# Optimization experiments

Measured on AMD Instinct MI355X. Metric: run time of the kernel, lower is better.

The kernel has to match this reference:

```python
import jax, jax.numpy as jnp
import numpy as np

B, S, D, H = 2, 2048, 1024, 16
HD = D // H  # head_dim = 64


def setup_inputs() -> dict:
    key = jax.random.key(0)
    k1, k2, k3, k4, k5 = jax.random.split(key, 5)
    x = jax.random.normal(k1, (B, S, D), dtype=jnp.float32)
    # causal additive mask [S, S]: 0 on/below diagonal, -1e9 above
    mask = jnp.where(jnp.tril(jnp.ones((S, S), dtype=bool)), 0.0, -1e9).astype(jnp.float32)
    scale = 1.0 / np.sqrt(D)
    W_qkv = jax.random.normal(k2, (D, 3 * D), dtype=jnp.float32) * scale
    b_qkv = jax.random.normal(k3, (3 * D,), dtype=jnp.float32) * 0.01
    W_o = jax.random.normal(k4, (D, D), dtype=jnp.float32) * scale
    b_o = jax.random.normal(k5, (D,), dtype=jnp.float32) * 0.01
    return {"x": x, "mask": mask, "W_qkv": W_qkv, "b_qkv": b_qkv, "W_o": W_o, "b_o": b_o}


def reference(x, mask, W_qkv, b_qkv, W_o, b_o):
    b, s, d = x.shape
    qkv = x @ W_qkv + b_qkv                         # [B,S,3D]
    qkv = qkv.reshape(b, s, H, 3 * HD).transpose(0, 2, 1, 3)  # [B,H,S,3*HD]
    q, k, v = jnp.split(qkv, 3, axis=-1)            # each [B,H,S,HD]
    scores = jnp.einsum('bhqd,bhkd->bhqk', q, k) / np.sqrt(HD)  # [B,H,S,S]
    scores = scores + mask                           # broadcast [S,S] additive mask
    attn = jax.nn.softmax(scores, axis=-1)
    vals = jnp.einsum('bhqk,bhkd->bhqd', attn, v)    # [B,H,S,HD]
    vals = vals.transpose(0, 2, 1, 3).reshape(b, s, d)
    return vals @ W_o + b_o
```

## Files before the change

### kernel.cpp

```cpp
#include <hip/hip_runtime.h>

#define NB 2
#define NS 2048
#define ND 1024
#define NH 16
#define NHD 64
#define QLD (3 * ND)
#define PADP 72

typedef unsigned short u16;
typedef __attribute__((ext_vector_type(8))) short short8;
typedef __attribute__((ext_vector_type(4))) float f32x4;

__device__ __forceinline__ u16 f2b(float f) {
    unsigned int x = __float_as_uint(f);
    return (u16)((x + 0x7fffu + ((x >> 16) & 1u)) >> 16);
}

__device__ __forceinline__ unsigned int cvtpk(float lo, float hi) {
    unsigned int r;
    asm("v_cvt_pk_bf16_f32 %0, %1, %2" : "=v"(r) : "v"(lo), "v"(hi));
    return r;
}

__device__ __forceinline__ int swz8(int d) {
    return ((d >> 1) ^ (d >> 3)) & 7;
}

__global__ __launch_bounds__(256) void prep(
    const float* __restrict__ x, u16* __restrict__ x_bf,
    const float* __restrict__ Wqkv, u16* __restrict__ WqkvT,
    const float* __restrict__ Wo, u16* __restrict__ WoT)
{
    __shared__ u16 Ts[64 * 72];
    const int bid = blockIdx.x;
    const int t = threadIdx.x;

    if (bid < 2048) {
        const int i = (bid * 256 + t) * 8;
        float4 a = *(const float4*)(x + i);
        float4 b = *(const float4*)(x + i + 4);
        *(ushort4*)(x_bf + i)     = make_ushort4(f2b(a.x), f2b(a.y), f2b(a.z), f2b(a.w));
        *(ushort4*)(x_bf + i + 4) = make_ushort4(f2b(b.x), f2b(b.y), f2b(b.z), f2b(b.w));
        return;
    }

    const float* W; u16* WT; int N, bx, by;
    if (bid < 2048 + 768) {
        const int r = bid - 2048;
        W = Wqkv; WT = WqkvT; N = QLD; bx = r % 48; by = r / 48;
    } else {
        const int r = bid - 2816;
        W = Wo; WT = WoT; N = ND; bx = r & 15; by = r >> 4;
    }
    const int K = ND;
    const int k0 = by << 6, n0 = bx << 6;
    const int rr0 = t >> 4, c = (t & 15) << 2;
    #pragma unroll
    for (int rr = 0; rr < 64; rr += 16) {
        float4 v = *(const float4*)&W[(size_t)(k0 + rr0 + rr) * N + n0 + c];
        Ts[(c + 0) * 72 + rr0 + rr] = f2b(v.x);
        Ts[(c + 1) * 72 + rr0 + rr] = f2b(v.y);
        Ts[(c + 2) * 72 + rr0 + rr] = f2b(v.z);
        Ts[(c + 3) * 72 + rr0 + rr] = f2b(v.w);
    }
    __syncthreads();
    const int n = t >> 2, cc = (t & 3) << 4;
    uint4 a = *(const uint4*)&Ts[n * 72 + cc];
    uint4 b = *(const uint4*)&Ts[n * 72 + cc + 8];
    *(uint4*)&WT[(size_t)(n0 + n) * K + k0 + cc]     = a;
    *(uint4*)&WT[(size_t)(n0 + n) * K + k0 + cc + 8] = b;
}

template <int BM, int BN, bool STORE_BF16>
__global__ __launch_bounds__(256) void gemm_mfma(
    const u16* __restrict__ A, const u16* __restrict__ BT,
    const float* __restrict__ bias,
    void* __restrict__ C, int M, int N, int K)
{
    constexpr int AIS = BM / 64;
    constexpr int BIS = BN / 64;
    constexpr int MI  = BM / 32;
    constexpr int NJ  = BN / 32;
    __shared__ u16 As[BM * 32];
    __shared__ u16 Bs[BN * 32];

    const int tid = threadIdx.x;
    const int wave = tid >> 6, lane = tid & 63;
    const int col = lane & 15, quad = lane >> 4;
    const int wm = wave >> 1, wn = wave & 1;

    const int nwgx = gridDim.x;
    const int wg = blockIdx.y * nwgx + blockIdx.x;
    const int cpx = (nwgx * gridDim.y) >> 3;
    const int swz = (wg & 7) * cpx + (wg >> 3);
    const int row0 = (swz / nwgx) * BM, col0 = (swz % nwgx) * BN;

    f32x4 acc[MI][NJ] = {};

    const u16* asrc[AIS];
    u16* adst[AIS];
    #pragma unroll
    for (int is = 0; is < AIS; ++is) {
        const int J = is * 256 + wave * 64 + lane;
        const int m = J >> 2;
        const int q = (J & 3) ^ ((m >> 1) & 3);
        asrc[is] = A + (size_t)(row0 + m) * K + q * 8;
        adst[is] = &As[(size_t)(is * 256 + wave * 64) * 8];
    }
    const u16* bsrc[BIS];
    u16* bdst[BIS];
    #pragma unroll
    for (int is = 0; is < BIS; ++is) {
        const int J = is * 256 + wave * 64 + lane;
        const int m = J >> 2;
        const int q = (J & 3) ^ ((m >> 1) & 3);
        bsrc[is] = BT + (size_t)(col0 + m) * K + q * 8;
        bdst[is] = &Bs[(size_t)(is * 256 + wave * 64) * 8];
    }

    for (int kk = 0; kk < K; kk += 32) {
        __syncthreads();
        #pragma unroll
        for (int is = 0; is < AIS; ++is)
            __builtin_amdgcn_global_load_lds(
                (const __attribute__((address_space(1))) unsigned int*)(asrc[is] + kk),
                (__attribute__((address_space(3))) unsigned int*)adst[is], 16, 0, 0);
        #pragma unroll
        for (int is = 0; is < BIS; ++is)
            __builtin_amdgcn_global_load_lds(
                (const __attribute__((address_space(1))) unsigned int*)(bsrc[is] + kk),
                (__attribute__((address_space(3))) unsigned int*)bdst[is], 16, 0, 0);
        __syncthreads();

        short8 af[MI], bf[NJ];
        #pragma unroll
        for (int i = 0; i < MI; ++i) {
            const int m = wm * (BM / 2) + i * 16 + col;
            af[i] = *(const short8*)&As[(m * 4 + (quad ^ ((m >> 1) & 3))) * 8];
        }
        #pragma unroll
        for (int j = 0; j < NJ; ++j) {
            const int n = wn * (BN / 2) + j * 16 + col;
            bf[j] = *(const short8*)&Bs[(n * 4 + (quad ^ ((n >> 1) & 3))) * 8];
        }
        #pragma unroll
        for (int i = 0; i < MI; ++i)
            #pragma unroll
            for (int j = 0; j < NJ; ++j)
                acc[i][j] = __builtin_amdgcn_mfma_f32_16x16x32_bf16(
                    af[i], bf[j], acc[i][j], 0, 0, 0);
    }

    #pragma unroll
    for (int j = 0; j < NJ; ++j) {
        const int gc = col0 + wn * (BN / 2) + j * 16 + col;
        const float bj = bias[gc];
        #pragma unroll
        for (int i = 0; i < MI; ++i) {
            const int gr = row0 + wm * (BM / 2) + i * 16 + quad * 4;
            #pragma unroll
            for (int r = 0; r < 4; ++r) {
                const float v = acc[i][j][r] + bj;
                if (STORE_BF16)
                    ((u16*)C)[(size_t)(gr + r) * N + gc] = f2b(v);
                else
                    ((float*)C)[(size_t)(gr + r) * N + gc] = v;
            }
        }
    }
}

__global__ __launch_bounds__(256) void attn_kernel(
    const u16* __restrict__ qkv, u16* __restrict__ vals)
{
    __shared__ u16 Ks[2][64 * 64];
    __shared__ u16 Vt[2][64 * 64];
    __shared__ u16 Ps[64 * PADP];

    const int tid = threadIdx.x;
    const int wave = tid >> 6, lane = tid & 63;
    const int col = lane & 15, quad = lane >> 4;
    const int qtA = blockIdx.x;
    const int qtB = 31 - qtA;
    const int bh = blockIdx.y;
    const int b = bh >> 4, h = bh & 15;
    const size_t base = (size_t)b * NS * QLD + (size_t)h * (3 * NHD);
    const int qloc = wave * 16 + col;

    int Jrow[2], Jcol[2];
    #pragma unroll
    for (int is = 0; is < 2; ++is) {
        const int J = is * 256 + wave * 64 + lane;
        Jrow[is] = J >> 3;
        Jcol[is] = ((J & 7) ^ (Jrow[is] & 7)) << 3;
    }

    auto stage_tile = [&](int buf, int srow, int coloff) {
        #pragma unroll
        for (int is = 0; is < 2; ++is) {
            __builtin_amdgcn_global_load_lds(
                (const __attribute__((address_space(1))) unsigned int*)
                    (qkv + base + (size_t)(srow + Jrow[is]) * QLD + coloff + Jcol[is]),
                (__attribute__((address_space(3))) unsigned int*)
                    &Ks[buf][(size_t)(is * 256 + wave * 64) * 8], 16, 0, 0);
        }
    };
    auto read_frag = [&](int buf, int row, int half) -> short8 {
        const int blk = row * 8 + ((quad + (half << 2)) ^ (row & 7));
        return *(const short8*)&Ks[buf][blk << 3];
    };

    const int vtx = tid & 15, vty = tid >> 4;
    const int vk0 = vty << 2, vd0 = vtx << 2;
    auto load_vregs = [&](int kt, ushort4* vr) {
        const u16* vsrc = qkv + base + (size_t)(kt * 64 + vk0) * QLD + 2 * NHD + vd0;
        vr[0] = *(const ushort4*)(vsrc);
        vr[1] = *(const ushort4*)(vsrc + QLD);
        vr[2] = *(const ushort4*)(vsrc + 2 * QLD);
        vr[3] = *(const ushort4*)(vsrc + 3 * QLD);
    };
    const int vC = vty >> 1, vS = (vty & 1) << 2;
    auto write_vt = [&](int buf, const ushort4* vr) {
        #pragma unroll
        for (int i = 0; i < 4; ++i) {
            const int d = vd0 + i;
            u16* p = &Vt[buf][d * 64 + ((vC ^ swz8(d)) << 3) + vS];
            *(ushort4*)p = make_ushort4(((const u16*)&vr[0])[i],
                                        ((const u16*)&vr[1])[i],
                                        ((const u16*)&vr[2])[i],
                                        ((const u16*)&vr[3])[i]);
        }
    };

    stage_tile(0, qtA * 64, 0);
    stage_tile(1, qtB * 64, 0);
    __syncthreads();
    short8 bqA0 = read_frag(0, qloc, 0), bqA1 = read_frag(0, qloc, 1);
    short8 bqB0 = read_frag(1, qloc, 0), bqB1 = read_frag(1, qloc, 1);
    __syncthreads();

    f32x4 accA[4] = {}, accB[4] = {};
    float mA = -1e30f, lA = 0.f, mB = -1e30f, lB = 0.f;

    auto qk = [&](const short8& b0, const short8& b1,
                  short8 (&kb)[4][2], f32x4 (&s)[4]) {
        __builtin_amdgcn_s_setprio(1);
        #pragma unroll
        for (int kg = 0; kg < 4; ++kg) {
            s[kg] = __builtin_amdgcn_mfma_f32_16x16x32_bf16(kb[kg][0], b0, s[kg], 0, 0, 0);
            s[kg] = __builtin_amdgcn_mfma_f32_16x16x32_bf16(kb[kg][1], b1, s[kg], 0, 0, 0);
        }
        __builtin_amdgcn_s_setprio(0);
    };

    auto sm = [&](f32x4 (&s)[4], f32x4 (&acc)[4], float& m, float& l, bool diag) {
        #pragma unroll
        for (int kg = 0; kg < 4; ++kg)
            #pragma unroll
            for (int r = 0; r < 4; ++r) {
                float v = s[kg][r] * 0.125f;
                if (diag && (kg * 16 + quad * 4 + r > qloc)) v = -1e30f;
                s[kg][r] = v;
            }
        float mx = -1e30f;
        #pragma unroll
        for (int kg = 0; kg < 4; ++kg)
            mx = fmaxf(mx, fmaxf(fmaxf(s[kg][0], s[kg][1]), fmaxf(s[kg][2], s[kg][3])));
        mx = fmaxf(mx, __shfl_xor(mx, 16, 64));
        mx = fmaxf(mx, __shfl_xor(mx, 32, 64));
        if (!__all(mx <= m + 8.f)) {
            const float mn = fmaxf(m, mx);
            const float alpha = __expf(m - mn);
            m = mn;
            l *= alpha;
            #pragma unroll
            for (int dg = 0; dg < 4; ++dg)
                #pragma unroll
                for (int r = 0; r < 4; ++r) acc[dg][r] *= alpha;
        }
        float psum = 0.f;
        #pragma unroll
        for (int kg = 0; kg < 4; ++kg) {
            float p0 = __expf(s[kg][0] - m);
            float p1 = __expf(s[kg][1] - m);
            float p2 = __expf(s[kg][2] - m);
            float p3 = __expf(s[kg][3] - m);
            psum += (p0 + p1) + (p2 + p3);
            uint2 w;
            w.x = cvtpk(p0, p1);
            w.y = cvtpk(p2, p3);
            *(uint2*)&Ps[qloc * PADP + kg * 16 + quad * 4] = w;
        }
        psum += __shfl_xor(psum, 16, 64);
        psum += __shfl_xor(psum, 32, 64);
        l += psum;
    };

    auto pv = [&](short8 (&vb)[4][2], f32x4 (&acc)[4]) {
        short8 pb0 = *(const short8*)&Ps[qloc * PADP + quad * 8];
        short8 pb1 = *(const short8*)&Ps[qloc * PADP + 32 + quad * 8];
        __builtin_amdgcn_s_setprio(1);
        #pragma unroll
        for (int dg = 0; dg < 4; ++dg) {
            acc[dg] = __builtin_amdgcn_mfma_f32_16x16x32_bf16(vb[dg][0], pb0, acc[dg], 0, 0, 0);
            acc[dg] = __builtin_amdgcn_mfma_f32_16x16x32_bf16(vb[dg][1], pb1, acc[dg], 0, 0, 0);
        }
        __builtin_amdgcn_s_setprio(0);
    };

    ushort4 vr[4];
    stage_tile(0, 0, NHD);
    load_vregs(0, vr);
    write_vt(0, vr);

    for (int kt = 0; kt <= qtB; ++kt) {
        const int cur = kt & 1, nxt = cur ^ 1;
        __syncthreads();
        if (kt < qtB) {
            stage_tile(nxt, (kt + 1) * 64, NHD);
            load_vregs(kt + 1, vr);
        }

        short8 kb[4][2], vb[4][2];
        #pragma unroll
        for (int kg = 0; kg < 4; ++kg) {
            kb[kg][0] = read_frag(cur, kg * 16 + col, 0);
            kb[kg][1] = read_frag(cur, kg * 16 + col, 1);
        }
        #pragma unroll
        for (int dg = 0; dg < 4; ++dg) {
            const int n = dg * 16 + col;
            #pragma unroll
            for (int c = 0; c < 2; ++c)
                vb[dg][c] = *(const short8*)
                    &Vt[cur][n * 64 + (((4 * c + quad) ^ swz8(n)) << 3)];
        }

        {
            f32x4 s[4] = {};
            qk(bqB0, bqB1, kb, s);
            sm(s, accB, mB, lB, kt == qtB);
            pv(vb, accB);
        }
        if (kt <= qtA) {
            f32x4 s[4] = {};
            qk(bqA0, bqA1, kb, s);
            sm(s, accA, mA, lA, kt == qtA);
            pv(vb, accA);
        }

        if (kt < qtB) write_vt(nxt, vr);
    }

    {
        const float inv = 1.f / lA;
        const size_t rowoff = ((size_t)b * NS + qtA * 64 + qloc) * ND + h * NHD;
        #pragma unroll
        for (int dg = 0; dg < 4; ++dg) {
            uint2 o;
            o.x = cvtpk(accA[dg][0] * inv, accA[dg][1] * inv);
            o.y = cvtpk(accA[dg][2] * inv, accA[dg][3] * inv);
            *(uint2*)(vals + rowoff + dg * 16 + quad * 4) = o;
        }
    }
    {
        const float inv = 1.f / lB;
        const size_t rowoff = ((size_t)b * NS + qtB * 64 + qloc) * ND + h * NHD;
        #pragma unroll
        for (int dg = 0; dg < 4; ++dg) {
            uint2 o;
            o.x = cvtpk(accB[dg][0] * inv, accB[dg][1] * inv);
            o.y = cvtpk(accB[dg][2] * inv, accB[dg][3] * inv);
            *(uint2*)(vals + rowoff + dg * 16 + quad * 4) = o;
        }
    }
}

extern "C" void kernel_launch(void* const* d_in, const int* in_sizes, int n_in,
                              void* d_out, int out_size, void* d_ws, size_t ws_size,
                              hipStream_t stream)
{
    const float* x    = (const float*)d_in[0];
    const float* Wqkv = (const float*)d_in[2];
    const float* bqkv = (const float*)d_in[3];
    const float* Wo   = (const float*)d_in[4];
    const float* bo   = (const float*)d_in[5];
    float* out = (float*)d_out;

    u16* x_bf   = (u16*)d_ws;
    u16* WqkvT  = x_bf   + (size_t)4096 * 1024;
    u16* WoT    = WqkvT  + (size_t)3072 * 1024;
    u16* qkv    = WoT    + (size_t)1024 * 1024;
    u16* vals   = qkv    + (size_t)4096 * 3072;

    const int M = NB * NS;

    prep<<<dim3(2048 + 768 + 256), dim3(256), 0, stream>>>(
        x, x_bf, Wqkv, WqkvT, Wo, WoT);

    gemm_mfma<128, 128, true><<<dim3(QLD / 128, M / 128), dim3(256), 0, stream>>>(
        x_bf, WqkvT, bqkv, qkv, M, QLD, ND);
    attn_kernel<<<dim3(16, NB * NH), dim3(256), 0, stream>>>(qkv, vals);
    gemm_mfma<64, 64, false><<<dim3(ND / 64, M / 64), dim3(256), 0, stream>>>(
        vals, WoT, bo, out, M, ND, ND);
}
```

Measured before the change: 202.6 us.

## Double-buffer GEMM LDS tiles, fold Q scaling into projection, defer softmax sum reduction

```diff
diff --git a/kernel.cpp b/kernel.cpp
--- a/kernel.cpp
+++ b/kernel.cpp
@@ -82,8 +82,8 @@
     constexpr int BIS = BN / 64;
     constexpr int MI  = BM / 32;
     constexpr int NJ  = BN / 32;
-    __shared__ u16 As[BM * 32];
-    __shared__ u16 Bs[BN * 32];
+    __shared__ u16 As[2][BM * 32];
+    __shared__ u16 Bs[2][BN * 32];
 
     const int tid = threadIdx.x;
     const int wave = tid >> 6, lane = tid & 63;
@@ -99,50 +99,59 @@
     f32x4 acc[MI][NJ] = {};
 
     const u16* asrc[AIS];
-    u16* adst[AIS];
+    u16* adst[2][AIS];
     #pragma unroll
     for (int is = 0; is < AIS; ++is) {
         const int J = is * 256 + wave * 64 + lane;
         const int m = J >> 2;
         const int q = (J & 3) ^ ((m >> 1) & 3);
         asrc[is] = A + (size_t)(row0 + m) * K + q * 8;
-        adst[is] = &As[(size_t)(is * 256 + wave * 64) * 8];
+        adst[0][is] = &As[0][(size_t)(is * 256 + wave * 64) * 8];
+        adst[1][is] = &As[1][(size_t)(is * 256 + wave * 64) * 8];
     }
     const u16* bsrc[BIS];
-    u16* bdst[BIS];
+    u16* bdst[2][BIS];
     #pragma unroll
     for (int is = 0; is < BIS; ++is) {
         const int J = is * 256 + wave * 64 + lane;
         const int m = J >> 2;
         const int q = (J & 3) ^ ((m >> 1) & 3);
         bsrc[is] = BT + (size_t)(col0 + m) * K + q * 8;
-        bdst[is] = &Bs[(size_t)(is * 256 + wave * 64) * 8];
-    }
-
-    for (int kk = 0; kk < K; kk += 32) {
-        __syncthreads();
+        bdst[0][is] = &Bs[0][(size_t)(is * 256 + wave * 64) * 8];
+        bdst[1][is] = &Bs[1][(size_t)(is * 256 + wave * 64) * 8];
+    }
+
+    auto stage = [&](int buf, int kk) {
         #pragma unroll
         for (int is = 0; is < AIS; ++is)
             __builtin_amdgcn_global_load_lds(
                 (const __attribute__((address_space(1))) unsigned int*)(asrc[is] + kk),
-                (__attribute__((address_space(3))) unsigned int*)adst[is], 16, 0, 0);
+                (__attribute__((address_space(3))) unsigned int*)adst[buf][is], 16, 0, 0);
         #pragma unroll
         for (int is = 0; is < BIS; ++is)
             __builtin_amdgcn_global_load_lds(
                 (const __attribute__((address_space(1))) unsigned int*)(bsrc[is] + kk),
-                (__attribute__((address_space(3))) unsigned int*)bdst[is], 16, 0, 0);
-        __syncthreads();
+                (__attribute__((address_space(3))) unsigned int*)bdst[buf][is], 16, 0, 0);
+    };
+
+    const int NT = K / 32;
+    stage(0, 0);
+    __syncthreads();
+
+    for (int t = 0; t < NT; ++t) {
+        const int cur = t & 1;
+        if (t + 1 < NT) stage(cur ^ 1, (t + 1) * 32);
 
         short8 af[MI], bf[NJ];
         #pragma unroll
         for (int i = 0; i < MI; ++i) {
             const int m = wm * (BM / 2) + i * 16 + col;
-            af[i] = *(const short8*)&As[(m * 4 + (quad ^ ((m >> 1) & 3))) * 8];
+            af[i] = *(const short8*)&As[cur][(m * 4 + (quad ^ ((m >> 1) & 3))) * 8];
         }
         #pragma unroll
         for (int j = 0; j < NJ; ++j) {
             const int n = wn * (BN / 2) + j * 16 + col;
-            bf[j] = *(const short8*)&Bs[(n * 4 + (quad ^ ((n >> 1) & 3))) * 8];
+            bf[j] = *(const short8*)&Bs[cur][(n * 4 + (quad ^ ((n >> 1) & 3))) * 8];
         }
         #pragma unroll
         for (int i = 0; i < MI; ++i)
@@ -150,18 +159,21 @@
             for (int j = 0; j < NJ; ++j)
                 acc[i][j] = __builtin_amdgcn_mfma_f32_16x16x32_bf16(
                     af[i], bf[j], acc[i][j], 0, 0, 0);
+
+        if (t + 1 < NT) __syncthreads();
     }
 
     #pragma unroll
     for (int j = 0; j < NJ; ++j) {
         const int gc = col0 + wn * (BN / 2) + j * 16 + col;
+        const float qs = (STORE_BF16 && (((gc >> 6) % 3) == 0)) ? 0.125f : 1.0f;
         const float bj = bias[gc];
         #pragma unroll
         for (int i = 0; i < MI; ++i) {
             const int gr = row0 + wm * (BM / 2) + i * 16 + quad * 4;
             #pragma unroll
             for (int r = 0; r < 4; ++r) {
-                const float v = acc[i][j][r] + bj;
+                const float v = (acc[i][j][r] + bj) * qs;
                 if (STORE_BF16)
                     ((u16*)C)[(size_t)(gr + r) * N + gc] = f2b(v);
                 else
@@ -254,15 +266,14 @@
         __builtin_amdgcn_s_setprio(0);
     };
 
-    auto sm = [&](f32x4 (&s)[4], f32x4 (&acc)[4], float& m, float& l, bool diag) {
-        #pragma unroll
-        for (int kg = 0; kg < 4; ++kg)
+    auto sm = [&](f32x4 (&s)[4], f32x4 (&acc)[4], float& m, float& lsum, bool diag) {
+        if (diag) {
             #pragma unroll
-            for (int r = 0; r < 4; ++r) {
-                float v = s[kg][r] * 0.125f;
-                if (diag && (kg * 16 + quad * 4 + r > qloc)) v = -1e30f;
-                s[kg][r] = v;
-            }
+            for (int kg = 0; kg < 4; ++kg)
+                #pragma unroll
+                for (int r = 0; r < 4; ++r)
+                    if (kg * 16 + quad * 4 + r > qloc) s[kg][r] = -1e30f;
+        }
         float mx = -1e30f;
         #pragma unroll
         for (int kg = 0; kg < 4; ++kg)
@@ -273,7 +284,7 @@
             const float mn = fmaxf(m, mx);
             const float alpha = __expf(m - mn);
             m = mn;
-            l *= alpha;
+            lsum *= alpha;
             #pragma unroll
             for (int dg = 0; dg < 4; ++dg)
                 #pragma unroll
@@ -292,9 +303,7 @@
             w.y = cvtpk(p2, p3);
             *(uint2*)&Ps[qloc * PADP + kg * 16 + quad * 4] = w;
         }
-        psum += __shfl_xor(psum, 16, 64);
-        psum += __shfl_xor(psum, 32, 64);
-        l += psum;
+        lsum += psum;
     };
 
     auto pv = [&](short8 (&vb)[4][2], f32x4 (&acc)[4]) {
@@ -354,7 +363,8 @@
     }
 
     {
-        const float inv = 1.f / lA;
+        float l1 = lA + __shfl_xor(lA, 16, 64);
+        const float inv = 1.f / (l1 + __shfl_xor(l1, 32, 64));
         const size_t rowoff = ((size_t)b * NS + qtA * 64 + qloc) * ND + h * NHD;
         #pragma unroll
         for (int dg = 0; dg < 4; ++dg) {
@@ -365,7 +375,8 @@
         }
     }
     {
-        const float inv = 1.f / lB;
+        float l1 = lB + __shfl_xor(lB, 16, 64);
+        const float inv = 1.f / (l1 + __shfl_xor(l1, 32, 64));
         const size_t rowoff = ((size_t)b * NS + qtB * 64 + qloc) * ND + h * NHD;
         #pragma unroll
         for (int dg = 0; dg < 4; ++dg) {
```

After: 199.8 us. About the same (-1.4%).
